# Performance work log

Measured on AMD Instinct MI355X. Metric: run time of the kernel, lower is better.

The kernel has to match this reference:

```python
import jax, jax.numpy as jnp
import numpy as np

B, L, HID = 256, 4096, 128
INNER = 8
LR = 0.01  # INFERENCE_LR


def setup_inputs() -> dict:
    key = jax.random.key(0)
    k_h, k_w1, k_b1, k_w2, k_b2 = jax.random.split(key, 5)
    bound1 = 1.0 / np.sqrt(HID)
    bound2 = 1.0 / np.sqrt(INNER)
    return {
        "h": jax.random.normal(k_h, (B, L, HID), dtype=jnp.float32),
        "W1": jax.random.uniform(k_w1, (INNER, HID), jnp.float32, -bound1, bound1),
        "b1": jax.random.uniform(k_b1, (INNER,), jnp.float32, -bound1, bound1),
        "W2": jax.random.uniform(k_w2, (HID, INNER), jnp.float32, -bound2, bound2),
        "b2": jax.random.uniform(k_b2, (HID,), jnp.float32, -bound2, bound2),
    }


def reference(h, W1, b1, W2, b2):
    Bsz, Ls, H = h.shape
    ts = jnp.arange(0, Ls - 3, 2)  # SGD step positions (static)
    inv_h = 2.0 / H  # d(mean sq err)/d(pred) factor over H elements

    def per_batch(hb):  # hb: (L, H)
        ks = hb[ts]       # keys  h[b, t]
        vs = hb[ts + 1]   # values h[b, t+1]

        def step(carry, kv):
            w1, c1, w2, c2 = carry
            k, v = kv
            a = w1 @ k + c1                 # (inner,)
            r = jnp.maximum(a, 0.0)
            pred = w2 @ r + c2              # (H,)
            g = inv_h * (pred - v)          # dLoss/dpred
            dW2 = jnp.outer(g, r)
            db2 = g
            da = (w2.T @ g) * (a > 0)
            dW1 = jnp.outer(da, k)
            db1 = da
            return (w1 - LR * dW1, c1 - LR * db1,
                    w2 - LR * dW2, c2 - LR * db2), None

        (w1, c1, w2, c2), _ = jax.lax.scan(step, (W1, b1, W2, b2), (ks, vs))
        x = hb[-1]
        return w2 @ jnp.maximum(w1 @ x + c1, 0.0) + c2  # (H,)

    return jax.vmap(per_batch)(h)  # (B, H)
```

## Files before the change

### kernel.cpp

```cpp
#include <hip/hip_runtime.h>

#define LRC 0.01f
#define LSEQ 4096
#define HIDDIM 128

typedef float f32x2 __attribute__((ext_vector_type(2)));
typedef unsigned int u32x2 __attribute__((ext_vector_type(2)));

#define RL(x, L) __int_as_float(__builtin_amdgcn_readlane(__float_as_int(x), (L)))
#define RORADD(x, ctrl)                                                      \
  x += __int_as_float(__builtin_amdgcn_update_dpp(                           \
      0, __float_as_int(x), (ctrl), 0xf, 0xf, true))

__device__ __forceinline__ float allred4(float x0, float x1, float x2,
                                         float x3) {
  u32x2 s1 = __builtin_amdgcn_permlane32_swap(__float_as_uint(x0),
                                              __float_as_uint(x1), false, false);
  float z01 = __uint_as_float(s1.x) + __uint_as_float(s1.y);
  u32x2 s2 = __builtin_amdgcn_permlane32_swap(__float_as_uint(x2),
                                              __float_as_uint(x3), false, false);
  float z23 = __uint_as_float(s2.x) + __uint_as_float(s2.y);
  u32x2 s3 = __builtin_amdgcn_permlane16_swap(__float_as_uint(z01),
                                              __float_as_uint(z23), false, false);
  float y = __uint_as_float(s3.x) + __uint_as_float(s3.y);
  RORADD(y, 0x128); RORADD(y, 0x124); RORADD(y, 0x122); RORADD(y, 0x121);
  return y;
}

__device__ __forceinline__ float allred1(float x) {
  u32x2 s1 = __builtin_amdgcn_permlane32_swap(__float_as_uint(x),
                                              __float_as_uint(x), false, false);
  float z = __uint_as_float(s1.x) + __uint_as_float(s1.y);
  u32x2 s2 = __builtin_amdgcn_permlane16_swap(__float_as_uint(z),
                                              __float_as_uint(z), false, false);
  z = __uint_as_float(s2.x) + __uint_as_float(s2.y);
  RORADD(z, 0x128); RORADD(z, 0x124); RORADD(z, 0x122); RORADD(z, 0x121);
  return z;
}

#define BAR() asm volatile("s_waitcnt lgkmcnt(0)\n\ts_barrier" ::: "memory")

__global__ __launch_bounds__(128) void ttt_kernel(
    const float* __restrict__ h, const float* __restrict__ W1,
    const float* __restrict__ b1, const float* __restrict__ W2,
    const float* __restrict__ b2, float* __restrict__ out) {
  __shared__ __align__(16) float sm[80];
  const int b = blockIdx.x;
  const int tid = threadIdx.x;
  const int wv = tid >> 6;
  const int lane = tid & 63;
  const int g = lane >> 4;
  const int sig = ((g & 1) << 1) | (g >> 1);
  const int d0 = lane * 2;
  const float* __restrict__ hb = h + (size_t)b * (LSEQ * HIDDIM);

  if (wv == 0) {
    const float cneg = -(LRC * 2.0f / (float)HIDDIM);
    f32x2 w2v[8];
#pragma unroll
    for (int i = 0; i < 8; ++i) {
      w2v[i].x = W2[(size_t)d0 * 8 + i];
      w2v[i].y = W2[(size_t)(d0 + 1) * 8 + i];
    }
    f32x2 b2v = *(const f32x2*)(b2 + d0);
    float b1A = b1[sig], b1B = b1[4 + sig];
    f32x2 vS0 = *(const f32x2*)(hb + 1 * HIDDIM + d0);
    f32x2 vS1 = *(const f32x2*)(hb + 3 * HIDDIM + d0);
    f32x2 vS2 = *(const f32x2*)(hb + 5 * HIDDIM + d0);
    f32x2 vS3 = *(const f32x2*)(hb + 7 * HIDDIM + d0);
    float pGlx = 0.0f, pGly = 0.0f;
    float pR0 = 0, pR1 = 0, pR2 = 0, pR3 = 0, pR4 = 0, pR5 = 0, pR6 = 0,
          pR7 = 0;
    float dm2A = 0, dm2B = 0, dm1A = 0, dm1B = 0;

    BAR();

    auto CORE = [&](float aA, float aB, f32x2 vcur, float& daAo, float& daBo,
                    bool defer) {
      float rA = fmaxf(aA, 0.0f), rB = fmaxf(aB, 0.0f);
      float r0 = RL(rA, 0), r1 = RL(rA, 32), r2 = RL(rA, 16), r3 = RL(rA, 48);
      float r4 = RL(rB, 0), r5 = RL(rB, 32), r6 = RL(rB, 16), r7 = RL(rB, 48);
      float px0 = fmaf(w2v[0].x, r0, b2v.x), py0 = fmaf(w2v[0].y, r0, b2v.y);
      float px1 = w2v[1].x * r1, py1 = w2v[1].y * r1;
      px0 = fmaf(w2v[2].x, r2, px0); py0 = fmaf(w2v[2].y, r2, py0);
      px1 = fmaf(w2v[3].x, r3, px1); py1 = fmaf(w2v[3].y, r3, py1);
      px0 = fmaf(w2v[4].x, r4, px0); py0 = fmaf(w2v[4].y, r4, py0);
      px1 = fmaf(w2v[5].x, r5, px1); py1 = fmaf(w2v[5].y, r5, py1);
      px0 = fmaf(w2v[6].x, r6, px0); py0 = fmaf(w2v[6].y, r6, py0);
      px1 = fmaf(w2v[7].x, r7, px1); py1 = fmaf(w2v[7].y, r7, py1);
      float glx = (px0 + px1 - vcur.x) * cneg;
      float gly = (py0 + py1 - vcur.y) * cneg;
      float dp[8];
#pragma unroll
      for (int i = 0; i < 8; ++i) dp[i] = fmaf(w2v[i].x, glx, w2v[i].y * gly);
      float zA = allred4(dp[0], dp[1], dp[2], dp[3]);
      float zB = allred4(dp[4], dp[5], dp[6], dp[7]);
      daAo = (aA > 0.0f) ? zA : 0.0f;
      daBo = (aB > 0.0f) ? zB : 0.0f;
      if (!defer) {
        w2v[0].x = fmaf(glx, r0, w2v[0].x); w2v[0].y = fmaf(gly, r0, w2v[0].y);
        w2v[1].x = fmaf(glx, r1, w2v[1].x); w2v[1].y = fmaf(gly, r1, w2v[1].y);
        w2v[2].x = fmaf(glx, r2, w2v[2].x); w2v[2].y = fmaf(gly, r2, w2v[2].y);
        w2v[3].x = fmaf(glx, r3, w2v[3].x); w2v[3].y = fmaf(gly, r3, w2v[3].y);
        w2v[4].x = fmaf(glx, r4, w2v[4].x); w2v[4].y = fmaf(gly, r4, w2v[4].y);
        w2v[5].x = fmaf(glx, r5, w2v[5].x); w2v[5].y = fmaf(gly, r5, w2v[5].y);
        w2v[6].x = fmaf(glx, r6, w2v[6].x); w2v[6].y = fmaf(gly, r6, w2v[6].y);
        w2v[7].x = fmaf(glx, r7, w2v[7].x); w2v[7].y = fmaf(gly, r7, w2v[7].y);
        b2v.x += glx;
        b2v.y += gly;
      } else {
        pGlx = glx; pGly = gly;
        pR0 = r0; pR1 = r1; pR2 = r2; pR3 = r3;
        pR4 = r4; pR5 = r5; pR6 = r6; pR7 = r7;
      }
    };

    auto APPLY_PEND = [&]() {
      w2v[0].x = fmaf(pGlx, pR0, w2v[0].x); w2v[0].y = fmaf(pGly, pR0, w2v[0].y);
      w2v[1].x = fmaf(pGlx, pR1, w2v[1].x); w2v[1].y = fmaf(pGly, pR1, w2v[1].y);
      w2v[2].x = fmaf(pGlx, pR2, w2v[2].x); w2v[2].y = fmaf(pGly, pR2, w2v[2].y);
      w2v[3].x = fmaf(pGlx, pR3, w2v[3].x); w2v[3].y = fmaf(pGly, pR3, w2v[3].y);
      w2v[4].x = fmaf(pGlx, pR4, w2v[4].x); w2v[4].y = fmaf(pGly, pR4, w2v[4].y);
      w2v[5].x = fmaf(pGlx, pR5, w2v[5].x); w2v[5].y = fmaf(pGly, pR5, w2v[5].y);
      w2v[6].x = fmaf(pGlx, pR6, w2v[6].x); w2v[6].y = fmaf(pGly, pR6, w2v[6].y);
      w2v[7].x = fmaf(pGlx, pR7, w2v[7].x); w2v[7].y = fmaf(pGly, pR7, w2v[7].y);
      b2v.x += pGlx;
      b2v.y += pGly;
    };

    auto EPA = [&](int ep, int e) {
      const int tpo = ep * 16, kko = 32 + ep * 5, dao = 48 + ep * 16;
      int rv0 = 4 * e + 9;  if (rv0 > 4095) rv0 = 4095;
      int rv1 = 4 * e + 11; if (rv1 > 4095) rv1 = 4095;
      f32x2 vI0 = *(const f32x2*)(hb + (size_t)rv0 * HIDDIM + d0);
      f32x2 vI1 = *(const f32x2*)(hb + (size_t)rv1 * HIDDIM + d0);
      float tpPA = sm[tpo + sig], tpPB = sm[tpo + 4 + sig];
      float tpQA = sm[tpo + 8 + sig], tpQB = sm[tpo + 12 + sig];
      float kk1 = sm[kko], kk2 = sm[kko + 1], kk3 = sm[kko + 2],
            kk4 = sm[kko + 3], kk5 = sm[kko + 4];
      APPLY_PEND();
      float aA = fmaf(dm2A, kk1, fmaf(dm1A, kk2, tpPA + b1A));
      float aB = fmaf(dm2B, kk1, fmaf(dm1B, kk2, tpPB + b1B));
      float daPA, daPB;
      CORE(aA, aB, vS0, daPA, daPB, false);
      if ((lane & 15) == 0) { sm[dao + sig] = daPA; sm[dao + 4 + sig] = daPB; }
      b1A += daPA;
      b1B += daPB;
      float aQA = fmaf(dm2A, kk3, fmaf(dm1A, kk4, fmaf(daPA, kk5, tpQA + b1A)));
      float aQB = fmaf(dm2B, kk3, fmaf(dm1B, kk4, fmaf(daPB, kk5, tpQB + b1B)));
      float daQA, daQB;
      CORE(aQA, aQB, vS1, daQA, daQB, true);
      if ((lane & 15) == 0) { sm[dao + 8 + sig] = daQA; sm[dao + 12 + sig] = daQB; }
      b1A += daQA;
      b1B += daQB;
      dm2A = daPA; dm2B = daPB;
      dm1A = daQA; dm1B = daQB;
      vS0 = vS2; vS1 = vS3; vS2 = vI0; vS3 = vI1;
      BAR();
    };

    for (int pr = 0; pr < 511; ++pr) {
      EPA(0, 2 * pr);
      EPA(1, 2 * pr + 1);
    }
    EPA(0, 1022);
    {
      float tpPA = sm[16 + sig], tpPB = sm[20 + sig];
      float tpQA = sm[24 + sig], tpQB = sm[28 + sig];
      float kk1 = sm[37], kk2 = sm[38], kk3 = sm[39], kk4 = sm[40],
            kk5 = sm[41];
      APPLY_PEND();
      float aA = fmaf(dm2A, kk1, fmaf(dm1A, kk2, tpPA + b1A));
      float aB = fmaf(dm2B, kk1, fmaf(dm1B, kk2, tpPB + b1B));
      float daA, daB;
      CORE(aA, aB, vS0, daA, daB, false);
      b1A += daA;
      b1B += daB;
      float fA = fmaf(dm2A, kk3, fmaf(dm1A, kk4, fmaf(daA, kk5, tpQA + b1A)));
      float fB = fmaf(dm2B, kk3, fmaf(dm1B, kk4, fmaf(daB, kk5, tpQB + b1B)));
      float rA = fmaxf(fA, 0.0f), rB = fmaxf(fB, 0.0f);
      float r0 = RL(rA, 0), r1 = RL(rA, 32), r2 = RL(rA, 16), r3 = RL(rA, 48);
      float r4 = RL(rB, 0), r5 = RL(rB, 32), r6 = RL(rB, 16), r7 = RL(rB, 48);
      float ox = fmaf(w2v[0].x, r0, b2v.x), oy = fmaf(w2v[0].y, r0, b2v.y);
      ox = fmaf(w2v[1].x, r1, ox); oy = fmaf(w2v[1].y, r1, oy);
      ox = fmaf(w2v[2].x, r2, ox); oy = fmaf(w2v[2].y, r2, oy);
      ox = fmaf(w2v[3].x, r3, ox); oy = fmaf(w2v[3].y, r3, oy);
      ox = fmaf(w2v[4].x, r4, ox); oy = fmaf(w2v[4].y, r4, oy);
      ox = fmaf(w2v[5].x, r5, ox); oy = fmaf(w2v[5].y, r5, oy);
      ox = fmaf(w2v[6].x, r6, ox); oy = fmaf(w2v[6].y, r6, oy);
      ox = fmaf(w2v[7].x, r7, ox); oy = fmaf(w2v[7].y, r7, oy);
      f32x2 o = {ox, oy};
      *(f32x2*)(out + (size_t)b * HIDDIM + d0) = o;
    }
  } else {
    f32x2 w1v[8];
#pragma unroll
    for (int i = 0; i < 8; ++i)
      w1v[i] = *(const f32x2*)(W1 + i * HIDDIM + d0);
    f32x2 kR2 = *(const f32x2*)(hb + 0 * HIDDIM + d0);
    f32x2 kR3 = *(const f32x2*)(hb + 2 * HIDDIM + d0);
    f32x2 kR4 = *(const f32x2*)(hb + 4 * HIDDIM + d0);
    f32x2 kR5 = *(const f32x2*)(hb + 6 * HIDDIM + d0);
    f32x2 kR0 = kR2, kR1 = kR2;
    f32x2 kI0 = *(const f32x2*)(hb + 8 * HIDDIM + d0);
    f32x2 kI1 = *(const f32x2*)(hb + 10 * HIDDIM + d0);
    if (lane < 16) sm[64 + lane] = 0.0f;
    {
      float pa[8], pb[8];
#pragma unroll
      for (int i = 0; i < 8; ++i) {
        pa[i] = fmaf(w1v[i].x, kR2.x, w1v[i].y * kR2.y);
        pb[i] = fmaf(w1v[i].x, kR3.x, w1v[i].y * kR3.y);
      }
      float zA = allred4(pa[0], pa[1], pa[2], pa[3]);
      float zB = allred4(pa[4], pa[5], pa[6], pa[7]);
      float tA = allred4(pb[0], pb[1], pb[2], pb[3]);
      float tB = allred4(pb[4], pb[5], pb[6], pb[7]);
      float kk01 = allred1(fmaf(kR2.x, kR3.x, kR2.y * kR3.y));
      if ((lane & 15) == 0) {
        sm[0 + sig] = zA;   sm[4 + sig] = zB;
        sm[8 + sig] = tA;   sm[12 + sig] = tB;
      }
      if (lane < 4) sm[32 + lane] = 0.0f;
      if (lane == 0) sm[36] = kk01;
    }
    BAR();

    auto EPB = [&](int ep, int e) {
      const int dao = 48 + (1 - ep) * 16;
      const int tpo = (1 - ep) * 16, kko = 32 + (1 - ep) * 5;
      int m6 = 2 * e + 6, m7 = 2 * e + 7;
      int r6 = (m6 >= 2047) ? 4095 : 2 * m6;
      int r7 = (m7 >= 2047) ? 4095 : 2 * m7;
      f32x2 kN0 = *(const f32x2*)(hb + (size_t)r6 * HIDDIM + d0);
      f32x2 kN1 = *(const f32x2*)(hb + (size_t)r7 * HIDDIM + d0);
      float4 qa = *(float4*)&sm[dao], qb = *(float4*)&sm[dao + 4];
      float4 qc = *(float4*)&sm[dao + 8], qd = *(float4*)&sm[dao + 12];
      float c1 = fmaf(kR2.x, kR4.x, kR2.y * kR4.y);
      float c2 = fmaf(kR3.x, kR4.x, kR3.y * kR4.y);
      float c3 = fmaf(kR2.x, kR5.x, kR2.y * kR5.y);
      float c4 = fmaf(kR3.x, kR5.x, kR3.y * kR5.y);
      float c5 = fmaf(kR4.x, kR5.x, kR4.y * kR5.y);
      float ykk = allred4(c1, c2, c3, c4);
      float yk5 = allred1(c5);
      float daP[8] = {qa.x, qa.y, qa.z, qa.w, qb.x, qb.y, qb.z, qb.w};
      float daQ[8] = {qc.x, qc.y, qc.z, qc.w, qd.x, qd.y, qd.z, qd.w};
#pragma unroll
      for (int i = 0; i < 8; ++i) {
        w1v[i].x = fmaf(daP[i], kR0.x, w1v[i].x);
        w1v[i].y = fmaf(daP[i], kR0.y, w1v[i].y);
      }
#pragma unroll
      for (int i = 0; i < 8; ++i) {
        w1v[i].x = fmaf(daQ[i], kR1.x, w1v[i].x);
        w1v[i].y = fmaf(daQ[i], kR1.y, w1v[i].y);
      }
      float tp[8], tq[8];
#pragma unroll
      for (int i = 0; i < 8; ++i) {
        tp[i] = fmaf(w1v[i].x, kR4.x, w1v[i].y * kR4.y);
        tq[i] = fmaf(w1v[i].x, kR5.x, w1v[i].y * kR5.y);
      }
      float tA = allred4(tp[0], tp[1], tp[2], tp[3]);
      float tB = allred4(tp[4], tp[5], tp[6], tp[7]);
      float uA = allred4(tq[0], tq[1], tq[2], tq[3]);
      float uB = allred4(tq[4], tq[5], tq[6], tq[7]);
      if ((lane & 15) == 0) {
        sm[tpo + sig] = tA;      sm[tpo + 4 + sig] = tB;
        sm[tpo + 8 + sig] = uA;  sm[tpo + 12 + sig] = uB;
        sm[kko + sig] = ykk;
      }
      if (lane == 0) sm[kko + 4] = yk5;
      kR0 = kR2; kR1 = kR3; kR2 = kR4; kR3 = kR5;
      kR4 = kI0; kR5 = kI1; kI0 = kN0; kI1 = kN1;
      BAR();
    };

    for (int pr = 0; pr < 511; ++pr) {
      EPB(0, 2 * pr);
      EPB(1, 2 * pr + 1);
    }
    EPB(0, 1022);
  }
}

extern "C" void kernel_launch(void* const* d_in, const int* in_sizes, int n_in,
                              void* d_out, int out_size, void* d_ws, size_t ws_size,
                              hipStream_t stream) {
  const float* h  = (const float*)d_in[0];
  const float* W1 = (const float*)d_in[1];
  const float* b1 = (const float*)d_in[2];
  const float* W2 = (const float*)d_in[3];
  const float* b2 = (const float*)d_in[4];
  float* out = (float*)d_out;
  ttt_kernel<<<256, 128, 0, stream>>>(h, W1, b1, W2, b2, out);
}
```

Before: 533.1 us.

## Process four SGD steps per barrier epoch instead of two

Widens the two-wave producer/consumer pipeline so each epoch covers four inner SGD steps instead of two. The W1 wave now precomputes four projections and the full set of key cross-dot products, and the W2 wave solves the four-step dependency chain locally. The barrier count is halved, cutting synchronisation and LDS round-trip overhead per step. The price is more registers (key and value windows of 16 and 8 entries), longer FMA chains per step, and more cross-lane reductions per epoch.

```diff
diff --git a/kernel.cpp b/kernel.cpp
--- a/kernel.cpp
+++ b/kernel.cpp
@@ -27,24 +27,17 @@
   return y;
 }
 
-__device__ __forceinline__ float allred1(float x) {
-  u32x2 s1 = __builtin_amdgcn_permlane32_swap(__float_as_uint(x),
-                                              __float_as_uint(x), false, false);
-  float z = __uint_as_float(s1.x) + __uint_as_float(s1.y);
-  u32x2 s2 = __builtin_amdgcn_permlane16_swap(__float_as_uint(z),
-                                              __float_as_uint(z), false, false);
-  z = __uint_as_float(s2.x) + __uint_as_float(s2.y);
-  RORADD(z, 0x128); RORADD(z, 0x124); RORADD(z, 0x122); RORADD(z, 0x121);
-  return z;
+#define BAR() asm volatile("s_waitcnt lgkmcnt(0)\n\ts_barrier" ::: "memory")
+
+__device__ __forceinline__ float dot2(f32x2 a, f32x2 b) {
+  return fmaf(a.x, b.x, a.y * b.y);
 }
-
-#define BAR() asm volatile("s_waitcnt lgkmcnt(0)\n\ts_barrier" ::: "memory")
 
 __global__ __launch_bounds__(128) void ttt_kernel(
     const float* __restrict__ h, const float* __restrict__ W1,
     const float* __restrict__ b1, const float* __restrict__ W2,
     const float* __restrict__ b2, float* __restrict__ out) {
-  __shared__ __align__(16) float sm[80];
+  __shared__ __align__(16) float sm[192];
   const int b = blockIdx.x;
   const int tid = threadIdx.x;
   const int wv = tid >> 6;
@@ -52,6 +45,7 @@
   const int g = lane >> 4;
   const int sig = ((g & 1) << 1) | (g >> 1);
   const int d0 = lane * 2;
+  const bool rowlead = ((lane & 15) == 0);
   const float* __restrict__ hb = h + (size_t)b * (LSEQ * HIDDIM);
 
   if (wv == 0) {
@@ -64,16 +58,15 @@
     }
     f32x2 b2v = *(const f32x2*)(b2 + d0);
     float b1A = b1[sig], b1B = b1[4 + sig];
-    f32x2 vS0 = *(const f32x2*)(hb + 1 * HIDDIM + d0);
-    f32x2 vS1 = *(const f32x2*)(hb + 3 * HIDDIM + d0);
-    f32x2 vS2 = *(const f32x2*)(hb + 5 * HIDDIM + d0);
-    f32x2 vS3 = *(const f32x2*)(hb + 7 * HIDDIM + d0);
+    f32x2 vS[8];
+#pragma unroll
+    for (int x = 0; x < 8; ++x)
+      vS[x] = *(const f32x2*)(hb + (size_t)(2 * x + 1) * HIDDIM + d0);
     float pGlx = 0.0f, pGly = 0.0f;
     float pR0 = 0, pR1 = 0, pR2 = 0, pR3 = 0, pR4 = 0, pR5 = 0, pR6 = 0,
           pR7 = 0;
-    float dm2A = 0, dm2B = 0, dm1A = 0, dm1B = 0;
-
-    BAR();
+    float dP0A = 0, dP1A = 0, dP2A = 0, dP3A = 0;
+    float dP0B = 0, dP1B = 0, dP2B = 0, dP3B = 0;
 
     auto CORE = [&](float aA, float aB, f32x2 vcur, float& daAo, float& daBo,
                     bool defer) {
@@ -114,7 +107,6 @@
         pR4 = r4; pR5 = r5; pR6 = r6; pR7 = r7;
       }
     };
-
     auto APPLY_PEND = [&]() {
       w2v[0].x = fmaf(pGlx, pR0, w2v[0].x); w2v[0].y = fmaf(pGly, pR0, w2v[0].y);
       w2v[1].x = fmaf(pGlx, pR1, w2v[1].x); w2v[1].y = fmaf(pGly, pR1, w2v[1].y);
@@ -128,56 +120,117 @@
       b2v.y += pGly;
     };
 
-    auto EPA = [&](int ep, int e) {
-      const int tpo = ep * 16, kko = 32 + ep * 5, dao = 48 + ep * 16;
-      int rv0 = 4 * e + 9;  if (rv0 > 4095) rv0 = 4095;
-      int rv1 = 4 * e + 11; if (rv1 > 4095) rv1 = 4095;
+    BAR();
+
+    for (int e = 0; e < 511; ++e) {
+      const int bb = (e & 1) * 96;
+      float tp0A = sm[bb + sig],      tp0B = sm[bb + 4 + sig];
+      float4 c0 = *(float4*)&sm[bb + 32];
+      float tp1A = sm[bb + 8 + sig],  tp1B = sm[bb + 12 + sig];
+      float4 c1 = *(float4*)&sm[bb + 40];
+      float  c1e = sm[bb + 44];
+      float tp2A = sm[bb + 16 + sig], tp2B = sm[bb + 20 + sig];
+      float4 c2 = *(float4*)&sm[bb + 48];
+      float2 c2e = *(float2*)&sm[bb + 52];
+      float tp3A = sm[bb + 24 + sig], tp3B = sm[bb + 28 + sig];
+      float4 c3 = *(float4*)&sm[bb + 56];
+      float2 c3e = *(float2*)&sm[bb + 60];
+      float  c3f = sm[bb + 62];
+      int rv0 = 8 * e + 17; if (rv0 > 4095) rv0 = 4095;
+      int rv1 = 8 * e + 19; if (rv1 > 4095) rv1 = 4095;
+      int rv2 = 8 * e + 21; if (rv2 > 4095) rv2 = 4095;
+      int rv3 = 8 * e + 23; if (rv3 > 4095) rv3 = 4095;
       f32x2 vI0 = *(const f32x2*)(hb + (size_t)rv0 * HIDDIM + d0);
       f32x2 vI1 = *(const f32x2*)(hb + (size_t)rv1 * HIDDIM + d0);
-      float tpPA = sm[tpo + sig], tpPB = sm[tpo + 4 + sig];
-      float tpQA = sm[tpo + 8 + sig], tpQB = sm[tpo + 12 + sig];
-      float kk1 = sm[kko], kk2 = sm[kko + 1], kk3 = sm[kko + 2],
-            kk4 = sm[kko + 3], kk5 = sm[kko + 4];
+      f32x2 vI2 = *(const f32x2*)(hb + (size_t)rv2 * HIDDIM + d0);
+      f32x2 vI3 = *(const f32x2*)(hb + (size_t)rv3 * HIDDIM + d0);
       APPLY_PEND();
-      float aA = fmaf(dm2A, kk1, fmaf(dm1A, kk2, tpPA + b1A));
-      float aB = fmaf(dm2B, kk1, fmaf(dm1B, kk2, tpPB + b1B));
-      float daPA, daPB;
-      CORE(aA, aB, vS0, daPA, daPB, false);
-      if ((lane & 15) == 0) { sm[dao + sig] = daPA; sm[dao + 4 + sig] = daPB; }
-      b1A += daPA;
-      b1B += daPB;
-      float aQA = fmaf(dm2A, kk3, fmaf(dm1A, kk4, fmaf(daPA, kk5, tpQA + b1A)));
-      float aQB = fmaf(dm2B, kk3, fmaf(dm1B, kk4, fmaf(daPB, kk5, tpQB + b1B)));
-      float daQA, daQB;
-      CORE(aQA, aQB, vS1, daQA, daQB, true);
-      if ((lane & 15) == 0) { sm[dao + 8 + sig] = daQA; sm[dao + 12 + sig] = daQB; }
-      b1A += daQA;
-      b1B += daQB;
-      dm2A = daPA; dm2B = daPB;
-      dm1A = daQA; dm1B = daQB;
-      vS0 = vS2; vS1 = vS3; vS2 = vI0; vS3 = vI1;
+      float a0A = fmaf(dP0A, c0.x, fmaf(dP1A, c0.y,
+                  fmaf(dP2A, c0.z, fmaf(dP3A, c0.w, tp0A + b1A))));
+      float a0B = fmaf(dP0B, c0.x, fmaf(dP1B, c0.y,
+                  fmaf(dP2B, c0.z, fmaf(dP3B, c0.w, tp0B + b1B))));
+      float da0A, da0B;
+      CORE(a0A, a0B, vS[0], da0A, da0B, false);
+      if (rowlead) { sm[bb + 64 + sig] = da0A; sm[bb + 68 + sig] = da0B; }
+      b1A += da0A; b1B += da0B;
+      float a1A = fmaf(dP0A, c1.x, fmaf(dP1A, c1.y, fmaf(dP2A, c1.z,
+                  fmaf(dP3A, c1.w, fmaf(da0A, c1e, tp1A + b1A)))));
+      float a1B = fmaf(dP0B, c1.x, fmaf(dP1B, c1.y, fmaf(dP2B, c1.z,
+                  fmaf(dP3B, c1.w, fmaf(da0B, c1e, tp1B + b1B)))));
+      float da1A, da1B;
+      CORE(a1A, a1B, vS[1], da1A, da1B, false);
+      if (rowlead) { sm[bb + 72 + sig] = da1A; sm[bb + 76 + sig] = da1B; }
+      b1A += da1A; b1B += da1B;
+      float a2A = fmaf(dP0A, c2.x, fmaf(dP1A, c2.y, fmaf(dP2A, c2.z,
+                  fmaf(dP3A, c2.w, fmaf(da0A, c2e.x,
+                  fmaf(da1A, c2e.y, tp2A + b1A))))));
+      float a2B = fmaf(dP0B, c2.x, fmaf(dP1B, c2.y, fmaf(dP2B, c2.z,
+                  fmaf(dP3B, c2.w, fmaf(da0B, c2e.x,
+                  fmaf(da1B, c2e.y, tp2B + b1B))))));
+      float da2A, da2B;
+      CORE(a2A, a2B, vS[2], da2A, da2B, false);
+      if (rowlead) { sm[bb + 80 + sig] = da2A; sm[bb + 84 + sig] = da2B; }
+      b1A += da2A; b1B += da2B;
+      float a3A = fmaf(dP0A, c3.x, fmaf(dP1A, c3.y, fmaf(dP2A, c3.z,
+                  fmaf(dP3A, c3.w, fmaf(da0A, c3e.x, fmaf(da1A, c3e.y,
+                  fmaf(da2A, c3f, tp3A + b1A)))))));
+      float a3B = fmaf(dP0B, c3.x, fmaf(dP1B, c3.y, fmaf(dP2B, c3.z,
+                  fmaf(dP3B, c3.w, fmaf(da0B, c3e.x, fmaf(da1B, c3e.y,
+                  fmaf(da2B, c3f, tp3B + b1B)))))));
+      float da3A, da3B;
+      CORE(a3A, a3B, vS[3], da3A, da3B, true);
+      if (rowlead) { sm[bb + 88 + sig] = da3A; sm[bb + 92 + sig] = da3B; }
+      b1A += da3A; b1B += da3B;
+      dP0A = da0A; dP1A = da1A; dP2A = da2A; dP3A = da3A;
+      dP0B = da0B; dP1B = da1B; dP2B = da2B; dP3B = da3B;
+      vS[0] = vS[4]; vS[1] = vS[5]; vS[2] = vS[6]; vS[3] = vS[7];
+      vS[4] = vI0; vS[5] = vI1; vS[6] = vI2; vS[7] = vI3;
       BAR();
-    };
-
-    for (int pr = 0; pr < 511; ++pr) {
-      EPA(0, 2 * pr);
-      EPA(1, 2 * pr + 1);
-    }
-    EPA(0, 1022);
+    }
     {
-      float tpPA = sm[16 + sig], tpPB = sm[20 + sig];
-      float tpQA = sm[24 + sig], tpQB = sm[28 + sig];
-      float kk1 = sm[37], kk2 = sm[38], kk3 = sm[39], kk4 = sm[40],
-            kk5 = sm[41];
+      const int bb = 96;
+      float tp0A = sm[bb + sig],      tp0B = sm[bb + 4 + sig];
+      float4 c0 = *(float4*)&sm[bb + 32];
+      float tp1A = sm[bb + 8 + sig],  tp1B = sm[bb + 12 + sig];
+      float4 c1 = *(float4*)&sm[bb + 40];
+      float  c1e = sm[bb + 44];
+      float tp2A = sm[bb + 16 + sig], tp2B = sm[bb + 20 + sig];
+      float4 c2 = *(float4*)&sm[bb + 48];
+      float2 c2e = *(float2*)&sm[bb + 52];
+      float tp3A = sm[bb + 24 + sig], tp3B = sm[bb + 28 + sig];
+      float4 c3 = *(float4*)&sm[bb + 56];
+      float2 c3e = *(float2*)&sm[bb + 60];
+      float  c3f = sm[bb + 62];
       APPLY_PEND();
-      float aA = fmaf(dm2A, kk1, fmaf(dm1A, kk2, tpPA + b1A));
-      float aB = fmaf(dm2B, kk1, fmaf(dm1B, kk2, tpPB + b1B));
-      float daA, daB;
-      CORE(aA, aB, vS0, daA, daB, false);
-      b1A += daA;
-      b1B += daB;
-      float fA = fmaf(dm2A, kk3, fmaf(dm1A, kk4, fmaf(daA, kk5, tpQA + b1A)));
-      float fB = fmaf(dm2B, kk3, fmaf(dm1B, kk4, fmaf(daB, kk5, tpQB + b1B)));
+      float a0A = fmaf(dP0A, c0.x, fmaf(dP1A, c0.y,
+                  fmaf(dP2A, c0.z, fmaf(dP3A, c0.w, tp0A + b1A))));
+      float a0B = fmaf(dP0B, c0.x, fmaf(dP1B, c0.y,
+                  fmaf(dP2B, c0.z, fmaf(dP3B, c0.w, tp0B + b1B))));
+      float da0A, da0B;
+      CORE(a0A, a0B, vS[0], da0A, da0B, false);
+      b1A += da0A; b1B += da0B;
+      float a1A = fmaf(dP0A, c1.x, fmaf(dP1A, c1.y, fmaf(dP2A, c1.z,
+                  fmaf(dP3A, c1.w, fmaf(da0A, c1e, tp1A + b1A)))));
+      float a1B = fmaf(dP0B, c1.x, fmaf(dP1B, c1.y, fmaf(dP2B, c1.z,
+                  fmaf(dP3B, c1.w, fmaf(da0B, c1e, tp1B + b1B)))));
+      float da1A, da1B;
+      CORE(a1A, a1B, vS[1], da1A, da1B, false);
+      b1A += da1A; b1B += da1B;
+      float a2A = fmaf(dP0A, c2.x, fmaf(dP1A, c2.y, fmaf(dP2A, c2.z,
+                  fmaf(dP3A, c2.w, fmaf(da0A, c2e.x,
+                  fmaf(da1A, c2e.y, tp2A + b1A))))));
+      float a2B = fmaf(dP0B, c2.x, fmaf(dP1B, c2.y, fmaf(dP2B, c2.z,
+                  fmaf(dP3B, c2.w, fmaf(da0B, c2e.x,
+                  fmaf(da1B, c2e.y, tp2B + b1B))))));
+      float da2A, da2B;
+      CORE(a2A, a2B, vS[2], da2A, da2B, false);
+      b1A += da2A; b1B += da2B;
+      float fA = fmaf(dP0A, c3.x, fmaf(dP1A, c3.y, fmaf(dP2A, c3.z,
+                 fmaf(dP3A, c3.w, fmaf(da0A, c3e.x, fmaf(da1A, c3e.y,
+                 fmaf(da2A, c3f, tp3A + b1A)))))));
+      float fB = fmaf(dP0B, c3.x, fmaf(dP1B, c3.y, fmaf(dP2B, c3.z,
+                 fmaf(dP3B, c3.w, fmaf(da0B, c3e.x, fmaf(da1B, c3e.y,
+                 fmaf(da2B, c3f, tp3B + b1B)))))));
       float rA = fmaxf(fA, 0.0f), rB = fmaxf(fB, 0.0f);
       float r0 = RL(rA, 0), r1 = RL(rA, 32), r2 = RL(rA, 16), r3 = RL(rA, 48);
       float r4 = RL(rB, 0), r5 = RL(rB, 32), r6 = RL(rB, 16), r7 = RL(rB, 48);
@@ -197,90 +250,126 @@
 #pragma unroll
     for (int i = 0; i < 8; ++i)
       w1v[i] = *(const f32x2*)(W1 + i * HIDDIM + d0);
-    f32x2 kR2 = *(const f32x2*)(hb + 0 * HIDDIM + d0);
-    f32x2 kR3 = *(const f32x2*)(hb + 2 * HIDDIM + d0);
-    f32x2 kR4 = *(const f32x2*)(hb + 4 * HIDDIM + d0);
-    f32x2 kR5 = *(const f32x2*)(hb + 6 * HIDDIM + d0);
-    f32x2 kR0 = kR2, kR1 = kR2;
-    f32x2 kI0 = *(const f32x2*)(hb + 8 * HIDDIM + d0);
-    f32x2 kI1 = *(const f32x2*)(hb + 10 * HIDDIM + d0);
-    if (lane < 16) sm[64 + lane] = 0.0f;
+    f32x2 kW[16];
+#pragma unroll
+    for (int x = 0; x < 4; ++x) {
+      kW[4 + x] = *(const f32x2*)(hb + (size_t)(2 * x) * HIDDIM + d0);
+      kW[8 + x] = *(const f32x2*)(hb + (size_t)(8 + 2 * x) * HIDDIM + d0);
+      kW[12 + x] = *(const f32x2*)(hb + (size_t)(16 + 2 * x) * HIDDIM + d0);
+    }
+    kW[0] = kW[4]; kW[1] = kW[4]; kW[2] = kW[4]; kW[3] = kW[4];
+    if (lane < 32) { sm[32 + lane] = 0.0f; sm[96 + 64 + lane] = 0.0f; }
     {
-      float pa[8], pb[8];
+      float tp[8];
+#pragma unroll
+      for (int i = 0; i < 8; ++i) tp[i] = dot2(w1v[i], kW[4]);
+      float t0A = allred4(tp[0], tp[1], tp[2], tp[3]);
+      float t0B = allred4(tp[4], tp[5], tp[6], tp[7]);
+#pragma unroll
+      for (int i = 0; i < 8; ++i) tp[i] = dot2(w1v[i], kW[5]);
+      float t1A = allred4(tp[0], tp[1], tp[2], tp[3]);
+      float t1B = allred4(tp[4], tp[5], tp[6], tp[7]);
+#pragma unroll
+      for (int i = 0; i < 8; ++i) tp[i] = dot2(w1v[i], kW[6]);
+      float t2A = allred4(tp[0], tp[1], tp[2], tp[3]);
+      float t2B = allred4(tp[4], tp[5], tp[6], tp[7]);
+#pragma unroll
+      for (int i = 0; i < 8; ++i) tp[i] = dot2(w1v[i], kW[7]);
+      float t3A = allred4(tp[0], tp[1], tp[2], tp[3]);
+      float t3B = allred4(tp[4], tp[5], tp[6], tp[7]);
+      float y3 = allred4(dot2(kW[4], kW[5]), 0.0f, 0.0f, 0.0f);
+      float y5 = allred4(dot2(kW[4], kW[6]), dot2(kW[5], kW[6]), 0.0f, 0.0f);
+      float y7 = allred4(dot2(kW[4], kW[7]), dot2(kW[5], kW[7]),
+                         dot2(kW[6], kW[7]), 0.0f);
+      if (rowlead) {
+        sm[0 + sig] = t0A;  sm[4 + sig] = t0B;
+        sm[8 + sig] = t1A;  sm[12 + sig] = t1B;
+        sm[16 + sig] = t2A; sm[20 + sig] = t2B;
+        sm[24 + sig] = t3A; sm[28 + sig] = t3B;
+        sm[44 + sig] = y3;  sm[52 + sig] = y5;  sm[60 + sig] = y7;
+      }
+    }
+    BAR();
+
+    for (int f = 0; f < 511; ++f) {
+      const int bb = ((f + 1) & 1) * 96;
+      float4 q0 = *(float4*)&sm[bb + 64], q1 = *(float4*)&sm[bb + 68];
+      float4 q2 = *(float4*)&sm[bb + 72], q3 = *(float4*)&sm[bb + 76];
+      float4 q4 = *(float4*)&sm[bb + 80], q5 = *(float4*)&sm[bb + 84];
+      float4 q6 = *(float4*)&sm[bb + 88], q7 = *(float4*)&sm[bb + 92];
+      int m0 = 4 * f + 12;
+      int rr0 = (m0 + 0 >= 2047) ? 4095 : 2 * (m0 + 0);
+      int rr1 = (m0 + 1 >= 2047) ? 4095 : 2 * (m0 + 1);
+      int rr2 = (m0 + 2 >= 2047) ? 4095 : 2 * (m0 + 2);
+      int rr3 = (m0 + 3 >= 2047) ? 4095 : 2 * (m0 + 3);
+      f32x2 kN0 = *(const f32x2*)(hb + (size_t)rr0 * HIDDIM + d0);
+      f32x2 kN1 = *(const f32x2*)(hb + (size_t)rr1 * HIDDIM + d0);
+      f32x2 kN2 = *(const f32x2*)(hb + (size_t)rr2 * HIDDIM + d0);
+      f32x2 kN3 = *(const f32x2*)(hb + (size_t)rr3 * HIDDIM + d0);
+      float yq0 = allred4(dot2(kW[4], kW[8]), dot2(kW[5], kW[8]),
+                          dot2(kW[6], kW[8]), dot2(kW[7], kW[8]));
+      float yq2 = allred4(dot2(kW[4], kW[9]), dot2(kW[5], kW[9]),
+                          dot2(kW[6], kW[9]), dot2(kW[7], kW[9]));
+      float yq3 = allred4(dot2(kW[8], kW[9]), 0.0f, 0.0f, 0.0f);
+      float yq4 = allred4(dot2(kW[4], kW[10]), dot2(kW[5], kW[10]),
+                          dot2(kW[6], kW[10]), dot2(kW[7], kW[10]));
+      float yq5 = allred4(dot2(kW[8], kW[10]), dot2(kW[9], kW[10]), 0.0f, 0.0f);
+      float yq6 = allred4(dot2(kW[4], kW[11]), dot2(kW[5], kW[11]),
+                          dot2(kW[6], kW[11]), dot2(kW[7], kW[11]));
+      float yq7 = allred4(dot2(kW[8], kW[11]), dot2(kW[9], kW[11]),
+                          dot2(kW[10], kW[11]), 0.0f);
+      if (rowlead) {
+        sm[bb + 32 + sig] = yq0;
+        sm[bb + 40 + sig] = yq2;
+        sm[bb + 44 + sig] = yq3;
+        sm[bb + 48 + sig] = yq4;
+        sm[bb + 52 + sig] = yq5;
+        sm[bb + 56 + sig] = yq6;
+        sm[bb + 60 + sig] = yq7;
+      }
+      float dT0[8] = {q0.x, q0.y, q0.z, q0.w, q1.x, q1.y, q1.z, q1.w};
+      float dT1[8] = {q2.x, q2.y, q2.z, q2.w, q3.x, q3.y, q3.z, q3.w};
+      float dT2[8] = {q4.x, q4.y, q4.z, q4.w, q5.x, q5.y, q5.z, q5.w};
+      float dT3[8] = {q6.x, q6.y, q6.z, q6.w, q7.x, q7.y, q7.z, q7.w};
 #pragma unroll
       for (int i = 0; i < 8; ++i) {
-        pa[i] = fmaf(w1v[i].x, kR2.x, w1v[i].y * kR2.y);
-        pb[i] = fmaf(w1v[i].x, kR3.x, w1v[i].y * kR3.y);
-      }
-      float zA = allred4(pa[0], pa[1], pa[2], pa[3]);
-      float zB = allred4(pa[4], pa[5], pa[6], pa[7]);
-      float tA = allred4(pb[0], pb[1], pb[2], pb[3]);
-      float tB = allred4(pb[4], pb[5], pb[6], pb[7]);
-      float kk01 = allred1(fmaf(kR2.x, kR3.x, kR2.y * kR3.y));
-      if ((lane & 15) == 0) {
-        sm[0 + sig] = zA;   sm[4 + sig] = zB;
-        sm[8 + sig] = tA;   sm[12 + sig] = tB;
-      }
-      if (lane < 4) sm[32 + lane] = 0.0f;
-      if (lane == 0) sm[36] = kk01;
-    }
-    BAR();
-
-    auto EPB = [&](int ep, int e) {
-      const int dao = 48 + (1 - ep) * 16;
-      const int tpo = (1 - ep) * 16, kko = 32 + (1 - ep) * 5;
-      int m6 = 2 * e + 6, m7 = 2 * e + 7;
-      int r6 = (m6 >= 2047) ? 4095 : 2 * m6;
-      int r7 = (m7 >= 2047) ? 4095 : 2 * m7;
-      f32x2 kN0 = *(const f32x2*)(hb + (size_t)r6 * HIDDIM + d0);
-      f32x2 kN1 = *(const f32x2*)(hb + (size_t)r7 * HIDDIM + d0);
-      float4 qa = *(float4*)&sm[dao], qb = *(float4*)&sm[dao + 4];
-      float4 qc = *(float4*)&sm[dao + 8], qd = *(float4*)&sm[dao + 12];
-      float c1 = fmaf(kR2.x, kR4.x, kR2.y * kR4.y);
-      float c2 = fmaf(kR3.x, kR4.x, kR3.y * kR4.y);
-      float c3 = fmaf(kR2.x, kR5.x, kR2.y * kR5.y);
-      float c4 = fmaf(kR3.x, kR5.x, kR3.y * kR5.y);
-      float c5 = fmaf(kR4.x, kR5.x, kR4.y * kR5.y);
-      float ykk = allred4(c1, c2, c3, c4);
-      float yk5 = allred1(c5);
-      float daP[8] = {qa.x, qa.y, qa.z, qa.w, qb.x, qb.y, qb.z, qb.w};
-      float daQ[8] = {qc.x, qc.y, qc.z, qc.w, qd.x, qd.y, qd.z, qd.w};
-#pragma unroll
-      for (int i = 0; i < 8; ++i) {
-        w1v[i].x = fmaf(daP[i], kR0.x, w1v[i].x);
-        w1v[i].y = fmaf(daP[i], kR0.y, w1v[i].y);
-      }
-#pragma unroll
-      for (int i = 0; i < 8; ++i) {
-        w1v[i].x = fmaf(daQ[i], kR1.x, w1v[i].x);
-        w1v[i].y = fmaf(daQ[i], kR1.y, w1v[i].y);
-      }
-      float tp[8], tq[8];
-#pragma unroll
-      for (int i = 0; i < 8; ++i) {
-        tp[i] = fmaf(w1v[i].x, kR4.x, w1v[i].y * kR4.y);
-        tq[i] = fmaf(w1v[i].x, kR5.x, w1v[i].y * kR5.y);
-      }
-      float tA = allred4(tp[0], tp[1], tp[2], tp[3]);
-      float tB = allred4(tp[4], tp[5], tp[6], tp[7]);
-      float uA = allred4(tq[0], tq[1], tq[2], tq[3]);
-      float uB = allred4(tq[4], tq[5], tq[6], tq[7]);
-      if ((lane & 15) == 0) {
-        sm[tpo + sig] = tA;      sm[tpo + 4 + sig] = tB;
-        sm[tpo + 8 + sig] = uA;  sm[tpo + 12 + sig] = uB;
-        sm[kko + sig] = ykk;
-      }
-      if (lane == 0) sm[kko + 4] = yk5;
-      kR0 = kR2; kR1 = kR3; kR2 = kR4; kR3 = kR5;
-      kR4 = kI0; kR5 = kI1; kI0 = kN0; kI1 = kN1;
+        w1v[i].x = fmaf(dT0[i], kW[0].x, w1v[i].x);
+        w1v[i].y = fmaf(dT0[i], kW[0].y, w1v[i].y);
+        w1v[i].x = fmaf(dT1[i], kW[1].x, w1v[i].x);
+        w1v[i].y = fmaf(dT1[i], kW[1].y, w1v[i].y);
+        w1v[i].x = fmaf(dT2[i], kW[2].x, w1v[i].x);
+        w1v[i].y = fmaf(dT2[i], kW[2].y, w1v[i].y);
+        w1v[i].x = fmaf(dT3[i], kW[3].x, w1v[i].x);
+        w1v[i].y = fmaf(dT3[i], kW[3].y, w1v[i].y);
+      }
+      float tp[8];
+#pragma unroll
+      for (int i = 0; i < 8; ++i) tp[i] = dot2(w1v[i], kW[8]);
+      float t0A = allred4(tp[0], tp[1], tp[2], tp[3]);
+      float t0B = allred4(tp[4], tp[5], tp[6], tp[7]);
+#pragma unroll
+      for (int i = 0; i < 8; ++i) tp[i] = dot2(w1v[i], kW[9]);
+      float t1A = allred4(tp[0], tp[1], tp[2], tp[3]);
+      float t1B = allred4(tp[4], tp[5], tp[6], tp[7]);
+#pragma unroll
+      for (int i = 0; i < 8; ++i) tp[i] = dot2(w1v[i], kW[10]);
+      float t2A = allred4(tp[0], tp[1], tp[2], tp[3]);
+      float t2B = allred4(tp[4], tp[5], tp[6], tp[7]);
+#pragma unroll
+      for (int i = 0; i < 8; ++i) tp[i] = dot2(w1v[i], kW[11]);
+      float t3A = allred4(tp[0], tp[1], tp[2], tp[3]);
+      float t3B = allred4(tp[4], tp[5], tp[6], tp[7]);
+      if (rowlead) {
+        sm[bb + 0 + sig] = t0A;  sm[bb + 4 + sig] = t0B;
+        sm[bb + 8 + sig] = t1A;  sm[bb + 12 + sig] = t1B;
+        sm[bb + 16 + sig] = t2A; sm[bb + 20 + sig] = t2B;
+        sm[bb + 24 + sig] = t3A; sm[bb + 28 + sig] = t3B;
+      }
+#pragma unroll
+      for (int i = 0; i < 12; ++i) kW[i] = kW[i + 4];
+      kW[12] = kN0; kW[13] = kN1; kW[14] = kN2; kW[15] = kN3;
       BAR();
-    };
-
-    for (int pr = 0; pr < 511; ++pr) {
-      EPB(0, 2 * pr);
-      EPB(1, 2 * pr + 1);
-    }
-    EPB(0, 1022);
+    }
   }
 }
 
```

Measured after the change: 551.9 us. 1.04x slower.
